# Kernel optimization log

Measured on AMD Instinct MI355X. Metric: run time of the kernel, lower is better.

The kernel has to match this reference:

```python
import jax, jax.numpy as jnp
import numpy as np

B, S, D_MODEL = 2, 2048, 2048
N_HEADS, N_KV = 32, 8
HEAD_DIM = D_MODEL // N_HEADS          # 64
HPG = N_HEADS // N_KV                  # heads per group = 4
DIM_K = HEAD_DIM * N_KV                # 512 (used as softmax scale per original code)


def setup_inputs() -> dict:
    key = jax.random.key(0)
    ks = jax.random.split(key, 11)
    s = lambda fan_in: 1.0 / np.sqrt(fan_in)
    return {
        "inputs_q": jax.random.normal(ks[0], (B, S, D_MODEL), jnp.float32),
        "inputs_k": jax.random.normal(ks[1], (B, S, D_MODEL), jnp.float32),
        "inputs_v": jax.random.normal(ks[2], (B, S, D_MODEL), jnp.float32),
        "Wq": jax.random.normal(ks[3], (D_MODEL, D_MODEL), jnp.float32) * s(D_MODEL),
        "bq": jnp.zeros((D_MODEL,), jnp.float32),
        "Wk": jax.random.normal(ks[4], (D_MODEL, DIM_K), jnp.float32) * s(D_MODEL),
        "bk": jnp.zeros((DIM_K,), jnp.float32),
        "Wv": jax.random.normal(ks[5], (D_MODEL, DIM_K), jnp.float32) * s(D_MODEL),
        "bv": jnp.zeros((DIM_K,), jnp.float32),
        "Wo": jax.random.normal(ks[6], (D_MODEL, D_MODEL), jnp.float32) * s(D_MODEL),
        "bo": jnp.zeros((D_MODEL,), jnp.float32),
    }


def reference(inputs_q, inputs_k, inputs_v, Wq, bq, Wk, bk, Wv, bv, Wo, bo):
    b, s, _ = inputs_q.shape
    q = inputs_q @ Wq + bq                       # [B,S,dim_q]
    k = inputs_k @ Wk + bk                       # [B,S,dim_k]
    v = inputs_v @ Wv + bv                       # [B,S,dim_v]
    q = q.reshape(b, s, N_KV, HPG, HEAD_DIM)     # b m g p d
    k = k.reshape(b, s, N_KV, HEAD_DIM)          # b n g d
    v = v.reshape(b, s, N_KV, HEAD_DIM)          # b n g d
    # logits[b,g,p,m,n] = q . k ; scale by sqrt(dim_k) per original code
    logits = jnp.einsum('bmgpd,bngd->bgpmn', q, k) / jnp.sqrt(jnp.float32(DIM_K))
    # causal mask (lower triangular allowed)
    causal = jnp.tril(jnp.ones((s, s), bool))
    logits = jnp.where(causal, logits, -jnp.inf)
    attn = jax.nn.softmax(logits, axis=-1)       # [B,G,P,M,N]
    out = jnp.einsum('bgpmn,bngd->bmgpd', attn, v)
    out = out.reshape(b, s, N_KV * HPG * HEAD_DIM)
    return out @ Wo + bo
```

## Files before the change

kernel.cpp:

```cpp
#include <hip/hip_runtime.h>
#include <hip/hip_bf16.h>

typedef __hip_bfloat16 bf16;
typedef float f32x4 __attribute__((ext_vector_type(4)));
typedef float f32x16 __attribute__((ext_vector_type(16)));
typedef short bf16x8 __attribute__((ext_vector_type(8)));

#define B_   2
#define S_   2048
#define DM   2048
#define HD   64
#define NH   32

__device__ __forceinline__ void async16(void* lds, const void* g) {
  __builtin_amdgcn_global_load_lds(
      (const __attribute__((address_space(1))) unsigned int*)g,
      (__attribute__((address_space(3))) unsigned int*)lds, 16, 0, 0);
}

template <int N> __device__ __forceinline__ void waitvm() {
  asm volatile("s_waitcnt vmcnt(%0)" :: "i"(N) : "memory");
}

__device__ __forceinline__ float exp2a(float x) {
  float r; asm("v_exp_f32 %0, %1" : "=v"(r) : "v"(x)); return r;
}
__device__ __forceinline__ unsigned cvtpk(float lo, float hi) {
  unsigned r; asm("v_cvt_pk_bf16_f32 %0, %1, %2" : "=v"(r) : "v"(lo), "v"(hi)); return r;
}
__device__ __forceinline__ void perm32swap(unsigned &a, unsigned &b) {
  asm volatile("v_permlane32_swap_b32 %0, %1" : "+v"(a), "+v"(b));
}

__global__ __launch_bounds__(256)
void prep_kernel(const float* __restrict__ xq, const float* __restrict__ xk,
                 const float* __restrict__ xv,
                 const float* __restrict__ Wq, const float* __restrict__ Wo,
                 const float* __restrict__ Wk, const float* __restrict__ Wv,
                 const float* __restrict__ bk, const float* __restrict__ bv,
                 bf16* __restrict__ Xq, bf16* __restrict__ Xk, bf16* __restrict__ Xv,
                 bf16* __restrict__ WqT, bf16* __restrict__ WoT, bf16* __restrict__ WkvT,
                 float* __restrict__ bkv) {
  const int blk = blockIdx.x;
  const int tid = threadIdx.x;

  if (blk < 12288) {
    const int a = blk >> 12;
    const int r = blk & 4095;
    const float* in = (a == 0) ? xq : (a == 1) ? xk : xv;
    bf16* out = (a == 0) ? Xq : (a == 1) ? Xk : Xv;
    const size_t i = ((size_t)r * 256 + tid) * 8;
    float4 v0 = *(const float4*)(in + i);
    float4 v1 = *(const float4*)(in + i + 4);
    union { bf16 h[8]; uint4 v; } u;
    u.h[0] = __float2bfloat16(v0.x); u.h[1] = __float2bfloat16(v0.y);
    u.h[2] = __float2bfloat16(v0.z); u.h[3] = __float2bfloat16(v0.w);
    u.h[4] = __float2bfloat16(v1.x); u.h[5] = __float2bfloat16(v1.y);
    u.h[6] = __float2bfloat16(v1.z); u.h[7] = __float2bfloat16(v1.w);
    *(uint4*)(out + i) = u.v;
    return;
  }

  int t = blk - 12288;
  const float* W; bf16* Wt; int N;
  if (t < 4096)       { W = Wq; Wt = WqT; N = 2048; }
  else if (t < 8192)  { t -= 4096; W = Wo; Wt = WoT; N = 2048; }
  else if (t < 9216)  { t -= 8192; W = Wk; Wt = WkvT; N = 512; }
  else if (t < 10240) { t -= 9216; W = Wv; Wt = WkvT + (size_t)512 * 2048; N = 512; }
  else {
    #pragma unroll
    for (int j = 0; j < 4; ++j) {
      const int i = tid * 4 + j;
      bkv[i] = (i < 512) ? bk[i] : bv[i - 512];
    }
    return;
  }
  const int k0 = (t & 63) * 32, n0 = (t >> 6) * 32;
  __shared__ float tile[32][33];
  const int tx = tid & 31, ty = tid >> 5;
  #pragma unroll
  for (int i = 0; i < 32; i += 8)
    tile[ty + i][tx] = W[(size_t)(k0 + ty + i) * N + n0 + tx];
  __syncthreads();
  #pragma unroll
  for (int i = 0; i < 32; i += 8)
    Wt[(size_t)(n0 + ty + i) * 2048 + k0 + tx] = __float2bfloat16(tile[tx][ty + i]);
}

__device__ __forceinline__ void store_out(float* C, size_t idx, float v) { C[idx] = v; }
__device__ __forceinline__ void store_out(bf16* C, size_t idx, float v) { C[idx] = __float2bfloat16(v); }

template <typename OUT>
__device__ __forceinline__ void gemm_body(const bf16* __restrict__ Au,
                                          const bf16* __restrict__ Bt,
                                          const float* __restrict__ bias, float omul,
                                          OUT* __restrict__ C, int N, int m0, int n0,
                                          bf16* As, bf16* Bs) {
  constexpr int BK = 32;
  const int tid = threadIdx.x;
  const int wave = tid >> 6, lane = tid & 63;
  const int l15 = lane & 15, l4 = lane >> 4;
  const int wm = (wave & 1) * 64, wn = (wave >> 1) * 64;

  f32x4 acc[4][4] = {};
  const int nk = 2048 / BK;

  auto stage = [&](int kt, int buf) {
    const int k0 = kt * BK;
    #pragma unroll
    for (int i = 0; i < 2; ++i) {
      const int rb = wave * 32 + i * 16;
      const int r  = rb + (lane >> 2);
      const int cs = (lane & 3) ^ ((r >> 1) & 3);
      async16(As + buf * 4096 + rb * BK, Au + (size_t)(m0 + r) * 2048 + k0 + cs * 8);
      async16(Bs + buf * 4096 + rb * BK, Bt + (size_t)(n0 + r) * 2048 + k0 + cs * 8);
    }
  };

  stage(0, 0);
  asm volatile("s_waitcnt vmcnt(0)" ::: "memory");
  __syncthreads();

  for (int kt = 0; kt < nk; ++kt) {
    const int cur = kt & 1;
    if (kt + 1 < nk) stage(kt + 1, cur ^ 1);
    bf16x8 af[4], bfr[4];
    #pragma unroll
    for (int f = 0; f < 4; ++f) {
      const int mr = wm + f * 16 + l15;
      af[f]  = *(const bf16x8*)(As + cur * 4096 + mr * BK + (l4 ^ ((mr >> 1) & 3)) * 8);
      const int nr = wn + f * 16 + l15;
      bfr[f] = *(const bf16x8*)(Bs + cur * 4096 + nr * BK + (l4 ^ ((nr >> 1) & 3)) * 8);
    }
    __builtin_amdgcn_s_setprio(1);
    #pragma unroll
    for (int i = 0; i < 4; ++i)
      #pragma unroll
      for (int j = 0; j < 4; ++j)
        acc[i][j] = __builtin_amdgcn_mfma_f32_16x16x32_bf16(af[i], bfr[j], acc[i][j], 0, 0, 0);
    __builtin_amdgcn_s_setprio(0);
    asm volatile("s_waitcnt vmcnt(0)" ::: "memory");
    __syncthreads();
  }

  const int r0 = m0 + wm + l4 * 4;
  const int c0 = n0 + wn + l15;
  #pragma unroll
  for (int j = 0; j < 4; ++j) {
    const int col = c0 + j * 16;
    const float bb = bias[col];
    #pragma unroll
    for (int i = 0; i < 4; ++i)
      #pragma unroll
      for (int r = 0; r < 4; ++r)
        store_out(C, (size_t)(r0 + i * 16 + r) * N + col, (acc[i][j][r] + bb) * omul);
  }
}

__global__ __launch_bounds__(256)
void gemm_qkv(const bf16* __restrict__ Xq, const bf16* __restrict__ Xk,
              const bf16* __restrict__ Xv,
              const bf16* __restrict__ WqT, const bf16* __restrict__ WkvT,
              const float* __restrict__ bq, const float* __restrict__ bkv,
              bf16* __restrict__ Qb, bf16* __restrict__ KVb) {
  __shared__ __align__(16) bf16 As[2][128 * 32];
  __shared__ __align__(16) bf16 Bs[2][128 * 32];
  const int bid = blockIdx.x;
  const int wg = (bid & 7) * 96 + (bid >> 3);
  if (wg < 512) {
    gemm_body<bf16>(Xq, WqT, bq, 0.063758717f, Qb, 2048,
                    (wg & 31) * 128, (wg >> 5) * 128, &As[0][0], &Bs[0][0]);
  } else {
    const int b2 = wg - 512;
    const int m0 = (b2 & 31) * 128, n0 = (b2 >> 5) * 128;
    gemm_body<bf16>(n0 < 512 ? Xk : Xv, WkvT, bkv, 1.0f, KVb, 1024,
                    m0, n0, &As[0][0], &Bs[0][0]);
  }
}

__global__ __launch_bounds__(256)
void gemm_o(const bf16* __restrict__ AO, const bf16* __restrict__ WoT,
            const float* __restrict__ bo, float* __restrict__ out) {
  __shared__ __align__(16) bf16 As[2][128 * 32];
  __shared__ __align__(16) bf16 Bs[2][128 * 32];
  gemm_body<float>(AO, WoT, bo, 1.0f, out, 2048,
                   blockIdx.x * 128, blockIdx.y * 128, &As[0][0], &Bs[0][0]);
}

__global__ __launch_bounds__(256, 3)
void attn_kernel(const bf16* __restrict__ Q, const bf16* __restrict__ KV, bf16* __restrict__ O) {
  const int h = blockIdx.x & 31, b = blockIdx.x >> 5;
  const int qt = 15 - blockIdx.y;
  const int g = h >> 2;
  const int tid = threadIdx.x;
  const int wave = tid >> 6, lane = tid & 63;
  const int l31 = lane & 31, l5 = lane >> 5;

  __shared__ __align__(16) char smem[40960];
  bf16* KsBuf = (bf16*)smem;
  bf16* VtBuf = (bf16*)(smem + 24576);
  char* ob = smem + wave * 4608;

  const bf16* KVb = KV + (size_t)(b * S_) * 1024;
  const int kcol = g * HD;
  const int vcol = 512 + g * HD;
  const int kv2 = tid & 31, vd0 = (tid >> 5) * 8;

  auto stageK = [&](int buf, int kv0) {
    #pragma unroll
    for (int i2 = 0; i2 < 2; ++i2) {
      const int rb = wave * 16 + i2 * 8;
      const int r = rb + (lane >> 3);
      const int cs = (lane & 7) ^ (r & 7);
      async16(KsBuf + buf * 4096 + rb * 64, KVb + (size_t)(kv0 + r) * 1024 + kcol + cs * 8);
    }
  };
  auto writeV = [&](int buf, uint4 va, uint4 vb) {
    const unsigned short* a0 = (const unsigned short*)&va;
    const unsigned short* a1 = (const unsigned short*)&vb;
    char* base = (char*)VtBuf + buf * 8192;
    #pragma unroll
    for (int j = 0; j < 8; ++j) {
      unsigned val = (unsigned)a0[j] | ((unsigned)a1[j] << 16);
      const int d = vd0 + j;
      *(unsigned*)(base + d * 128 + ((kv2 * 4) ^ ((d & 7) << 4))) = val;
    }
  };

  const int qbase = qt * 128;
  const int nt = 2 * qt + 2;
  const int qrow = qbase + wave * 32 + l31;
  const int wmax = qbase + wave * 32 + 31;

  bf16x8 qf[4];
  const bf16* qp = Q + (size_t)(b * S_ + qrow) * DM + h * HD + l5 * 8;
  #pragma unroll
  for (int ks = 0; ks < 4; ++ks) qf[ks] = *(const bf16x8*)(qp + ks * 16);

  f32x16 ot[2] = {};
  float m = -3.0e38f, lsum = 0.f;
  uint4 vr0, vr1;

  {
    const bf16* vp = KVb + (size_t)(2 * kv2) * 1024 + vcol + vd0;
    vr0 = *(const uint4*)vp;
    vr1 = *(const uint4*)(vp + 1024);
  }
  stageK(0, 0);
  stageK(1, 64);
  waitvm<4>();
  writeV(0, vr0, vr1);
  waitvm<2>();
  asm volatile("s_waitcnt lgkmcnt(0)" ::: "memory");
  __builtin_amdgcn_s_barrier();
  asm volatile("" ::: "memory");

  for (int t = 0; t < nt; ++t) {
    const int kv0 = t * 64;
    if (t + 1 < nt) {
      const bf16* vp = KVb + (size_t)((t + 1) * 64 + 2 * kv2) * 1024 + vcol + vd0;
      vr0 = *(const uint4*)vp;
      vr1 = *(const uint4*)(vp + 1024);
    }
    if (t + 2 < nt) stageK((t + 2) % 3, (t + 2) * 64);

    if (kv0 <= wmax) {
      const char* kb = (const char*)(KsBuf + (t % 3) * 4096);
      const char* vb = (const char*)(VtBuf + (t & 1) * 4096);
      f32x16 sT[2] = {};
      __builtin_amdgcn_s_setprio(1);
      #pragma unroll
      for (int ks = 0; ks < 4; ++ks) {
        #pragma unroll
        for (int i = 0; i < 2; ++i) {
          const int row = i * 32 + l31;
          bf16x8 kf = *(const bf16x8*)(kb + row * 128 +
                                       ((ks * 32 + l5 * 16) ^ ((row & 7) << 4)));
          sT[i] = __builtin_amdgcn_mfma_f32_32x32x16_bf16(kf, qf[ks], sT[i], 0, 0, 0);
        }
      }
      __builtin_amdgcn_s_setprio(0);
      if (kv0 + 63 > qbase + wave * 32) {
        #pragma unroll
        for (int i = 0; i < 2; ++i)
          #pragma unroll
          for (int r = 0; r < 16; ++r) {
            const int kvg = kv0 + i * 32 + ((r & 3) + 8 * (r >> 2)) + 4 * l5;
            if (kvg > qrow) sT[i][r] = -3.0e38f;
          }
      }
      float a16[16];
      #pragma unroll
      for (int r = 0; r < 16; ++r) a16[r] = fmaxf(sT[0][r], sT[1][r]);
      #pragma unroll
      for (int s2 = 8; s2 >= 1; s2 >>= 1)
        #pragma unroll
        for (int r = 0; r < 8; ++r) if (r < s2) a16[r] = fmaxf(a16[r], a16[r + s2]);
      float pm = fmaxf(a16[0], __shfl_xor(a16[0], 32));
      if (!__all(pm - m <= 8.f)) {
        const float mn = fmaxf(m, pm);
        const float alpha = exp2a(m - mn);
        m = mn;
        lsum *= alpha;
        #pragma unroll
        for (int r = 0; r < 16; ++r) { ot[0][r] *= alpha; ot[1][r] *= alpha; }
      }
      float rs0 = 0.f, rs1 = 0.f;
      unsigned pk[2][8];
      #pragma unroll
      for (int i = 0; i < 2; ++i)
        #pragma unroll
        for (int rr = 0; rr < 8; ++rr) {
          const float p0 = exp2a(sT[i][2 * rr] - m);
          const float p1 = exp2a(sT[i][2 * rr + 1] - m);
          if (i == 0) rs0 += p0 + p1; else rs1 += p0 + p1;
          pk[i][rr] = cvtpk(p0, p1);
        }
      float rs = rs0 + rs1;
      rs += __shfl_xor(rs, 32);
      lsum += rs;
      #pragma unroll
      for (int i = 0; i < 2; ++i) {
        #pragma unroll
        for (int kp = 0; kp < 2; ++kp) {
          unsigned w0 = pk[i][4 * kp + 0], w1 = pk[i][4 * kp + 1];
          unsigned w2 = pk[i][4 * kp + 2], w3 = pk[i][4 * kp + 3];
          perm32swap(w0, w2);
          perm32swap(w1, w3);
          union { unsigned u[4]; bf16x8 v; } pf = {{w0, w1, w2, w3}};
          const int ks2 = i * 2 + kp;
          __builtin_amdgcn_s_setprio(1);
          #pragma unroll
          for (int f = 0; f < 2; ++f) {
            const int row = f * 32 + l31;
            bf16x8 vf = *(const bf16x8*)(vb + row * 128 +
                                         ((ks2 * 32 + l5 * 16) ^ ((row & 7) << 4)));
            ot[f] = __builtin_amdgcn_mfma_f32_32x32x16_bf16(vf, pf.v, ot[f], 0, 0, 0);
          }
          __builtin_amdgcn_s_setprio(0);
        }
      }
    }

    if (t + 2 < nt) waitvm<2>();
    else            waitvm<0>();
    if (t + 1 < nt) writeV((t + 1) & 1, vr0, vr1);
    asm volatile("s_waitcnt lgkmcnt(0)" ::: "memory");
    __builtin_amdgcn_s_barrier();
    asm volatile("" ::: "memory");
  }

  const float inv = 1.0f / lsum;
  #pragma unroll
  for (int f = 0; f < 2; ++f)
    #pragma unroll
    for (int g2 = 0; g2 < 4; ++g2) {
      uint2 val;
      val.x = cvtpk(ot[f][g2 * 4 + 0] * inv, ot[f][g2 * 4 + 1] * inv);
      val.y = cvtpk(ot[f][g2 * 4 + 2] * inv, ot[f][g2 * 4 + 3] * inv);
      *(uint2*)(ob + l31 * 144 + f * 64 + g2 * 16 + l5 * 8) = val;
    }
  asm volatile("s_waitcnt lgkmcnt(0)" ::: "memory");
  __builtin_amdgcn_sched_barrier(0);
  #pragma unroll
  for (int rr = 0; rr < 4; ++rr) {
    const int row = rr * 8 + (lane >> 3);
    uint4 dv = *(const uint4*)(ob + row * 144 + (lane & 7) * 16);
    *(uint4*)(O + (size_t)(b * S_ + qbase + wave * 32 + row) * DM + h * HD + (lane & 7) * 8) = dv;
  }
}

extern "C" void kernel_launch(void* const* d_in, const int* in_sizes, int n_in,
                              void* d_out, int out_size, void* d_ws, size_t ws_size,
                              hipStream_t stream) {
  const float* xq = (const float*)d_in[0];
  const float* xk = (const float*)d_in[1];
  const float* xv = (const float*)d_in[2];
  const float* Wq = (const float*)d_in[3];
  const float* bq = (const float*)d_in[4];
  const float* Wk = (const float*)d_in[5];
  const float* bk = (const float*)d_in[6];
  const float* Wv = (const float*)d_in[7];
  const float* bv = (const float*)d_in[8];
  const float* Wo = (const float*)d_in[9];
  const float* bo = (const float*)d_in[10];
  float* out = (float*)d_out;

  char* ws = (char*)d_ws;
  bf16*  Xq   = (bf16*)(ws);
  bf16*  Xk   = (bf16*)(ws + 16777216);
  bf16*  Xv   = (bf16*)(ws + 33554432);
  bf16*  WqT  = (bf16*)(ws + 50331648);
  bf16*  WkvT = (bf16*)(ws + 58720256);
  bf16*  WoT  = (bf16*)(ws + 62914560);
  float* bkv  = (float*)(ws + 71303168);
  bf16*  Qb   = (bf16*)(ws + 71307264);
  bf16*  KVb  = (bf16*)(ws + 88084480);
  bf16*  AO   = Xq;

  prep_kernel<<<22529, 256, 0, stream>>>(xq, xk, xv, Wq, Wo, Wk, Wv, bk, bv,
                                         Xq, Xk, Xv, WqT, WoT, WkvT, bkv);
  gemm_qkv<<<768, 256, 0, stream>>>(Xq, Xk, Xv, WqT, WkvT, bq, bkv, Qb, KVb);
  attn_kernel<<<dim3(64, 16), 256, 0, stream>>>(Qb, KVb, AO);
  gemm_o<<<dim3(32, 16), 256, 0, stream>>>(AO, WoT, bo, out);
}
```

Before: 223.0 us.

## Use 256x256 tiles with 512 threads for the QKV projection GEMM

```diff
diff --git a/kernel.cpp b/kernel.cpp
--- a/kernel.cpp
+++ b/kernel.cpp
@@ -157,24 +157,100 @@
   }
 }
 
-__global__ __launch_bounds__(256)
+__device__ __forceinline__ void gemm256_body(const bf16* __restrict__ Au,
+                                             const bf16* __restrict__ Bt,
+                                             const float* __restrict__ bias, float omul,
+                                             bf16* __restrict__ C, int N, int m0, int n0,
+                                             char* smem) {
+  char* AsB = smem;
+  char* BsB = smem + 65536;
+  const int tid = threadIdx.x;
+  const int wave = tid >> 6, lane = tid & 63;
+  const int l15 = lane & 15, l4 = lane >> 4;
+  const int wr = wave >> 2, wc = wave & 3;
+
+  f32x4 acc[8][4] = {};
+
+  auto stage = [&](int buf, int kt) {
+    const int k0 = kt * 64;
+    #pragma unroll
+    for (int i = 0; i < 4; ++i) {
+      const int rb = wave * 32 + i * 8;
+      const int r = rb + (lane >> 3);
+      const int cs = (lane & 7) ^ (r & 7);
+      async16(AsB + buf * 32768 + rb * 128, Au + (size_t)(m0 + r) * 2048 + k0 + cs * 8);
+      async16(BsB + buf * 32768 + rb * 128, Bt + (size_t)(n0 + r) * 2048 + k0 + cs * 8);
+    }
+  };
+
+  stage(0, 0);
+  waitvm<0>();
+  __builtin_amdgcn_s_barrier();
+  asm volatile("" ::: "memory");
+
+  for (int kt = 0; kt < 32; ++kt) {
+    const int cur = kt & 1;
+    if (kt + 1 < 32) stage(cur ^ 1, kt + 1);
+    const char* ab = AsB + cur * 32768;
+    const char* bb = BsB + cur * 32768;
+    #pragma unroll
+    for (int ks = 0; ks < 2; ++ks) {
+      bf16x8 af[8], bg[4];
+      #pragma unroll
+      for (int mf = 0; mf < 8; ++mf) {
+        const int row = wr * 128 + mf * 16 + l15;
+        af[mf] = *(const bf16x8*)(ab + row * 128 + (((ks * 4 + l4) ^ (row & 7)) << 4));
+      }
+      #pragma unroll
+      for (int nf = 0; nf < 4; ++nf) {
+        const int row = wc * 64 + nf * 16 + l15;
+        bg[nf] = *(const bf16x8*)(bb + row * 128 + (((ks * 4 + l4) ^ (row & 7)) << 4));
+      }
+      __builtin_amdgcn_s_setprio(1);
+      #pragma unroll
+      for (int mf = 0; mf < 8; ++mf)
+        #pragma unroll
+        for (int nf = 0; nf < 4; ++nf)
+          acc[mf][nf] = __builtin_amdgcn_mfma_f32_16x16x32_bf16(af[mf], bg[nf],
+                                                                acc[mf][nf], 0, 0, 0);
+      __builtin_amdgcn_s_setprio(0);
+    }
+    waitvm<0>();
+    __builtin_amdgcn_s_barrier();
+    asm volatile("" ::: "memory");
+  }
+
+  const int r0 = m0 + wr * 128 + l4 * 4;
+  const int c0 = n0 + wc * 64 + l15;
+  #pragma unroll
+  for (int nf = 0; nf < 4; ++nf) {
+    const int col = c0 + nf * 16;
+    const float bb2 = bias[col];
+    #pragma unroll
+    for (int mf = 0; mf < 8; ++mf)
+      #pragma unroll
+      for (int r = 0; r < 4; ++r)
+        C[(size_t)(r0 + mf * 16 + r) * N + col] =
+            __float2bfloat16((acc[mf][nf][r] + bb2) * omul);
+  }
+}
+
+__global__ __launch_bounds__(512, 2)
 void gemm_qkv(const bf16* __restrict__ Xq, const bf16* __restrict__ Xk,
               const bf16* __restrict__ Xv,
               const bf16* __restrict__ WqT, const bf16* __restrict__ WkvT,
               const float* __restrict__ bq, const float* __restrict__ bkv,
               bf16* __restrict__ Qb, bf16* __restrict__ KVb) {
-  __shared__ __align__(16) bf16 As[2][128 * 32];
-  __shared__ __align__(16) bf16 Bs[2][128 * 32];
+  __shared__ __align__(16) char smem[131072];
   const int bid = blockIdx.x;
-  const int wg = (bid & 7) * 96 + (bid >> 3);
-  if (wg < 512) {
-    gemm_body<bf16>(Xq, WqT, bq, 0.063758717f, Qb, 2048,
-                    (wg & 31) * 128, (wg >> 5) * 128, &As[0][0], &Bs[0][0]);
+  const int wgid = (bid & 7) * 24 + (bid >> 3);
+  const int m0 = (wgid & 15) * 256;
+  const int ng = wgid >> 4;
+  if (ng < 8) {
+    gemm256_body(Xq, WqT, bq, 0.063758717f, Qb, 2048, m0, ng * 256, smem);
   } else {
-    const int b2 = wg - 512;
-    const int m0 = (b2 & 31) * 128, n0 = (b2 >> 5) * 128;
-    gemm_body<bf16>(n0 < 512 ? Xk : Xv, WkvT, bkv, 1.0f, KVb, 1024,
-                    m0, n0, &As[0][0], &Bs[0][0]);
+    const int n0 = (ng - 8) * 256;
+    gemm256_body(n0 < 512 ? Xk : Xv, WkvT, bkv, 1.0f, KVb, 1024, m0, n0, smem);
   }
 }
 
@@ -400,7 +476,7 @@
 
   prep_kernel<<<22529, 256, 0, stream>>>(xq, xk, xv, Wq, Wo, Wk, Wv, bk, bv,
                                          Xq, Xk, Xv, WqT, WoT, WkvT, bkv);
-  gemm_qkv<<<768, 256, 0, stream>>>(Xq, Xk, Xv, WqT, WkvT, bq, bkv, Qb, KVb);
+  gemm_qkv<<<192, 512, 0, stream>>>(Xq, Xk, Xv, WqT, WkvT, bq, bkv, Qb, KVb);
   attn_kernel<<<dim3(64, 16), 256, 0, stream>>>(Qb, KVb, AO);
   gemm_o<<<dim3(32, 16), 256, 0, stream>>>(AO, WoT, bo, out);
 }
```

Measured after the change: 210.0 us. -5.8%, faster.
